# Optimization experiments

Measured on AMD Instinct MI355X. Metric: run time of the kernel, lower is better.

## Reference

```python
import jax, jax.numpy as jnp
import numpy as np

N_NODES = 50000
N_EDGES = 1600000
IN_FEAT = 48
OUT_FEAT = 48
NUM_RELS = 8


def setup_inputs() -> dict:
    key = jax.random.key(0)
    ks = jax.random.split(key, 9)
    # xavier-ish scale for relu gain
    s1 = float(np.sqrt(2.0) * np.sqrt(6.0 / (IN_FEAT + IN_FEAT)))
    s2 = float(np.sqrt(2.0) * np.sqrt(6.0 / (IN_FEAT + OUT_FEAT)))
    return {
        "inputs": jax.random.normal(ks[0], (N_NODES, IN_FEAT), dtype=jnp.float32),
        "norm": jax.random.uniform(ks[1], (N_EDGES, 1), dtype=jnp.float32),
        "weight1": jax.random.uniform(ks[2], (NUM_RELS, IN_FEAT, IN_FEAT), jnp.float32, -s1, s1),
        "weight2": jax.random.uniform(ks[3], (NUM_RELS, IN_FEAT, OUT_FEAT), jnp.float32, -s2, s2),
        "bias1": jax.random.normal(ks[4], (IN_FEAT,), dtype=jnp.float32) * 0.1,
        "bias2": jax.random.normal(ks[5], (OUT_FEAT,), dtype=jnp.float32) * 0.1,
        "src": jax.random.randint(ks[6], (N_EDGES,), 0, N_NODES, dtype=jnp.int64) if jax.config.jax_enable_x64 else jax.random.randint(ks[6], (N_EDGES,), 0, N_NODES).astype(jnp.int32),
        "dst": jax.random.randint(ks[7], (N_EDGES,), 0, N_NODES).astype(jnp.int32),
        "rel_type": jax.random.randint(ks[8], (N_EDGES,), 0, NUM_RELS).astype(jnp.int32),
    }


def reference(inputs, norm, weight1, weight2, bias1, bias2, src, dst, rel_type):
    # Message depends only on (src node, relation): precompute per (node, rel).
    # Stage 1: h1[n,r,:] = relu(h[n] @ W1[r] + b1)   -> [N, R, in]
    h1 = jax.nn.relu(jnp.einsum('ni,rij->nrj', inputs, weight1) + bias1)
    # Stage 2: h2[n,r,:] = h1[n,r] @ W2[r]           -> [N, R, out]
    h2 = jnp.einsum('nrj,rjo->nro', h1, weight2)
    # Per-edge gather + norm scaling                 -> [E, out]
    msg = h2[src, rel_type] * norm
    # Scatter-sum aggregation to destination nodes   -> [N, out]
    agg = jax.ops.segment_sum(msg, dst, num_segments=inputs.shape[0])
    # apply_func: bias2 + activation
    return jax.nn.relu(agg + bias2)
```

## Files before the change

### kernel.cpp

```cpp
#include <hip/hip_runtime.h>

#define NN 50000
#define EE 1600000
#define FF 48
#define RR 8
#define H2_ROW 64
#define LSTR 72
#define NSEG 8
#define SCAP 16

#define WB 8

#define H2TILES 391
#define H2BLKS (H2TILES * RR)
#define K2GRID (H2BLKS * 3)

typedef __attribute__((ext_vector_type(8))) short frag8;
typedef __attribute__((ext_vector_type(4))) float frag4f;

__device__ inline unsigned short bf16r(float f) {
    unsigned u = __float_as_uint(f);
    return (unsigned short)((u + 0x7FFFu + ((u >> 16) & 1u)) >> 16);
}
__device__ inline unsigned bf16pack2(float a, float b) {
    return (unsigned)bf16r(a) | ((unsigned)bf16r(b) << 16);
}
__device__ inline frag8 pack8(float4 a, float4 b) {
    union { frag8 f; unsigned u[4]; } r;
    r.u[0] = bf16pack2(a.x, a.y); r.u[1] = bf16pack2(a.z, a.w);
    r.u[2] = bf16pack2(b.x, b.y); r.u[3] = bf16pack2(b.z, b.w);
    return r.f;
}

__global__ __launch_bounds__(256) void pre_kernel(
    const float* __restrict__ W1, const float* __restrict__ W2,
    unsigned short* __restrict__ W1t, unsigned short* __restrict__ W2t)
{
    int r = blockIdx.x;
    const float* w1 = W1 + (size_t)r * FF * FF;
    const float* w2 = W2 + (size_t)r * FF * FF;
    for (int idx = threadIdx.x; idx < 48 * 64; idx += 256) {
        int j = idx >> 6, k = idx & 63;
        W1t[(size_t)r * 48 * 64 + idx] = (k < FF) ? bf16r(w1[k * FF + j]) : (unsigned short)0;
        W2t[(size_t)r * 48 * 64 + idx] = (k < FF) ? bf16r(w2[k * FF + j]) : (unsigned short)0;
    }
}

__global__ __launch_bounds__(256) void h2_place_kernel(
    const float* __restrict__ X, const unsigned short* __restrict__ W1t,
    const unsigned short* __restrict__ W2t, const float* __restrict__ B1,
    const int* __restrict__ srcv, const int* __restrict__ dstv,
    const int* __restrict__ relv, const float* __restrict__ norm,
    int* __restrict__ count, unsigned* __restrict__ payload,
    unsigned short* __restrict__ H2)
{
    __shared__ unsigned short h1s[128 * LSTR];
    int b = blockIdx.x;
    int bmod = b - (b / 3) * 3;
    if (bmod != 0) {
        int p = (b / 3) * 2 + bmod - 1;
        int e = p * 256 + threadIdx.x;
        if (e < EE) {
            int xcd;
            asm volatile("s_getreg_b32 %0, hwreg(HW_REG_XCC_ID)" : "=s"(xcd));
            xcd &= (NSEG - 1);
            int d = dstv[e];
            unsigned qn = (unsigned)(norm[e] * 8192.0f + 0.5f);
            if (qn > 8191u) qn = 8191u;
            unsigned rec = ((unsigned)(srcv[e] * 8 + relv[e]) << 13) | qn;
            int x = xcd;
            #pragma unroll 1
            for (int attempt = 0; attempt < NSEG; ++attempt) {
                int pos = atomicAdd(&count[d * NSEG + x], 1);
                if (pos < SCAP) {
                    __builtin_nontemporal_store(
                        rec, &payload[((size_t)d * NSEG + x) * SCAP + pos]);
                    break;
                }
                x = (x + 1) & (NSEG - 1);
            }
        }
        return;
    }
    int h    = b / 3;
    int r    = h & 7;
    int tile = h >> 3;
    int tid  = threadIdx.x;
    int w    = tid >> 6, ln = tid & 63, q = ln >> 4, lq = ln & 15;
    int nb   = tile * 128 + w * 32;

    unsigned short* myh1 = &h1s[(w * 32) * LSTR];
    for (int i = ln; i < 32 * 12; i += 64) {
        int rr = i / 12, cs = i - rr * 12;
        *(unsigned*)&myh1[rr * LSTR + 48 + cs * 2] = 0;
    }

    int row0 = nb + lq;      if (row0 >= NN) row0 = NN - 1;
    int row1 = nb + 16 + lq; if (row1 >= NN) row1 = NN - 1;
    const float* x0 = X + (size_t)row0 * FF;
    const float* x1 = X + (size_t)row1 * FF;

    frag8 a00 = pack8(*(const float4*)(x0 + q * 8), *(const float4*)(x0 + q * 8 + 4));
    frag8 a10 = pack8(*(const float4*)(x1 + q * 8), *(const float4*)(x1 + q * 8 + 4));
    frag8 a01 = {0, 0, 0, 0, 0, 0, 0, 0};
    frag8 a11 = {0, 0, 0, 0, 0, 0, 0, 0};
    if (q < 2) {
        a01 = pack8(*(const float4*)(x0 + 32 + q * 8), *(const float4*)(x0 + 36 + q * 8));
        a11 = pack8(*(const float4*)(x1 + 32 + q * 8), *(const float4*)(x1 + 36 + q * 8));
    }

    const unsigned short* w1r = W1t + (size_t)r * 48 * 64;
    const unsigned short* w2r = W2t + (size_t)r * 48 * 64;

    #pragma unroll
    for (int t = 0; t < 3; ++t) {
        int col = t * 16 + lq;
        frag8 b0 = *(const frag8*)&w1r[(col << 6) + q * 8];
        frag8 b1 = *(const frag8*)&w1r[(col << 6) + 32 + q * 8];
        float bc = B1[col];
        frag4f acc0 = {bc, bc, bc, bc};
        frag4f acc1 = {bc, bc, bc, bc};
        acc0 = __builtin_amdgcn_mfma_f32_16x16x32_bf16(a00, b0, acc0, 0, 0, 0);
        acc0 = __builtin_amdgcn_mfma_f32_16x16x32_bf16(a01, b1, acc0, 0, 0, 0);
        acc1 = __builtin_amdgcn_mfma_f32_16x16x32_bf16(a10, b0, acc1, 0, 0, 0);
        acc1 = __builtin_amdgcn_mfma_f32_16x16x32_bf16(a11, b1, acc1, 0, 0, 0);
        #pragma unroll
        for (int g = 0; g < 4; ++g) {
            myh1[(q * 4 + g) * LSTR + col]      = bf16r(fmaxf(acc0[g], 0.0f));
            myh1[(16 + q * 4 + g) * LSTR + col] = bf16r(fmaxf(acc1[g], 0.0f));
        }
    }

    const frag8 c00 = *(const frag8*)&myh1[lq * LSTR + q * 8];
    const frag8 c01 = *(const frag8*)&myh1[lq * LSTR + 32 + q * 8];
    const frag8 c10 = *(const frag8*)&myh1[(16 + lq) * LSTR + q * 8];
    const frag8 c11 = *(const frag8*)&myh1[(16 + lq) * LSTR + 32 + q * 8];

    #pragma unroll
    for (int t = 0; t < 3; ++t) {
        int col = t * 16 + lq;
        frag8 b0 = *(const frag8*)&w2r[(col << 6) + q * 8];
        frag8 b1 = *(const frag8*)&w2r[(col << 6) + 32 + q * 8];
        frag4f acc0 = {0.f, 0.f, 0.f, 0.f};
        frag4f acc1 = {0.f, 0.f, 0.f, 0.f};
        acc0 = __builtin_amdgcn_mfma_f32_16x16x32_bf16(c00, b0, acc0, 0, 0, 0);
        acc0 = __builtin_amdgcn_mfma_f32_16x16x32_bf16(c01, b1, acc0, 0, 0, 0);
        acc1 = __builtin_amdgcn_mfma_f32_16x16x32_bf16(c10, b0, acc1, 0, 0, 0);
        acc1 = __builtin_amdgcn_mfma_f32_16x16x32_bf16(c11, b1, acc1, 0, 0, 0);
        #pragma unroll
        for (int g = 0; g < 4; ++g) {
            int n0 = nb + q * 4 + g;
            int n1 = nb + 16 + q * 4 + g;
            if (n0 < NN) H2[((size_t)n0 * RR + r) * H2_ROW + col] = bf16r(acc0[g]);
            if (n1 < NN) H2[((size_t)n1 * RR + r) * H2_ROW + col] = bf16r(acc1[g]);
        }
    }
}

__global__ __launch_bounds__(256) void gather_kernel(
    const unsigned short* __restrict__ H2, const unsigned* __restrict__ payload,
    const int* __restrict__ count, const float* __restrict__ B2,
    float* __restrict__ out)
{
    unsigned tid = blockIdx.x * 256u + threadIdx.x;
    unsigned n = tid / 12u;
    unsigned c = tid - n * 12u;
    if (n >= NN) return;

    int4 ca = ((const int4*)(count + (size_t)n * NSEG))[0];
    int4 cb = ((const int4*)(count + (size_t)n * NSEG))[1];
    int c0 = min(ca.x, SCAP), c1 = min(ca.y, SCAP);
    int c2 = min(ca.z, SCAP), c3 = min(ca.w, SCAP);
    int c4 = min(cb.x, SCAP), c5 = min(cb.y, SCAP);
    int c6 = min(cb.z, SCAP), c7 = min(cb.w, SCAP);
    int p1 = c0, p2 = p1 + c1, p3 = p2 + c2, p4 = p3 + c3;
    int p5 = p4 + c4, p6 = p5 + c5, p7 = p6 + c6;
    int total = p7 + c7;
    const unsigned* pl = payload + (size_t)n * (NSEG * SCAP);

    auto slot = [&](int idx) -> unsigned {
        int x, base;
        if (idx < p4) {
            if (idx < p2) { x = (idx < p1) ? 0 : 1; base = (idx < p1) ? 0 : p1; }
            else          { x = (idx < p3) ? 2 : 3; base = (idx < p3) ? p2 : p3; }
        } else {
            if (idx < p6) { x = (idx < p5) ? 4 : 5; base = (idx < p5) ? p4 : p5; }
            else          { x = (idx < p7) ? 6 : 7; base = (idx < p7) ? p6 : p7; }
        }
        return pl[x * SCAP + (idx - base)];
    };

    float a0 = 0.f, a1 = 0.f, a2 = 0.f, a3 = 0.f;
    int e = 0;
    for (; e + 8 <= total; e += 8) {
        unsigned p[8];
        #pragma unroll
        for (int k = 0; k < 8; ++k) p[k] = slot(e + k);
        uint2 v[8];
        #pragma unroll
        for (int k = 0; k < 8; ++k)
            v[k] = ((const uint2*)(H2 + (size_t)(p[k] >> 13) * H2_ROW))[c];
        #pragma unroll
        for (int k = 0; k < 8; ++k) {
            float nm = (float)(p[k] & 8191u) * (1.0f / 8192.0f);
            a0 = fmaf(__uint_as_float(v[k].x << 16),         nm, a0);
            a1 = fmaf(__uint_as_float(v[k].x & 0xFFFF0000u), nm, a1);
            a2 = fmaf(__uint_as_float(v[k].y << 16),         nm, a2);
            a3 = fmaf(__uint_as_float(v[k].y & 0xFFFF0000u), nm, a3);
        }
    }
    for (; e < total; ++e) {
        unsigned p = slot(e);
        float nm = (float)(p & 8191u) * (1.0f / 8192.0f);
        uint2 v = ((const uint2*)(H2 + (size_t)(p >> 13) * H2_ROW))[c];
        a0 = fmaf(__uint_as_float(v.x << 16),         nm, a0);
        a1 = fmaf(__uint_as_float(v.x & 0xFFFF0000u), nm, a1);
        a2 = fmaf(__uint_as_float(v.y << 16),         nm, a2);
        a3 = fmaf(__uint_as_float(v.y & 0xFFFF0000u), nm, a3);
    }
    float4 b = ((const float4*)B2)[c];
    ((float4*)out)[(size_t)n * 12u + c] = make_float4(
        fmaxf(a0 + b.x, 0.f), fmaxf(a1 + b.y, 0.f),
        fmaxf(a2 + b.z, 0.f), fmaxf(a3 + b.w, 0.f));
}

extern "C" void kernel_launch(void* const* d_in, const int* in_sizes, int n_in,
                              void* d_out, int out_size, void* d_ws, size_t ws_size,
                              hipStream_t stream) {
    const float* X   = (const float*)d_in[0];
    const float* nrm = (const float*)d_in[1];
    const float* W1  = (const float*)d_in[2];
    const float* W2  = (const float*)d_in[3];
    const float* B1  = (const float*)d_in[4];
    const float* B2  = (const float*)d_in[5];
    const int*   src = (const int*)d_in[6];
    const int*   dst = (const int*)d_in[7];
    const int*   rel = (const int*)d_in[8];
    float* out = (float*)d_out;

    unsigned short* H2      = (unsigned short*)d_ws;
    unsigned*       payload = (unsigned*)(H2 + (size_t)NN * RR * H2_ROW);
    unsigned short* W1t     = (unsigned short*)(payload + (size_t)NN * NSEG * SCAP);
    unsigned short* W2t     = W1t + RR * 48 * 64;
    int*            count   = (int*)(W2t + RR * 48 * 64);

    hipMemsetAsync(count, 0, (size_t)NN * NSEG * sizeof(int), stream);

    pre_kernel<<<WB, 256, 0, stream>>>(W1, W2, W1t, W2t);

    h2_place_kernel<<<K2GRID, 256, 0, stream>>>(
        X, W1t, W2t, B1, src, dst, rel, nrm, count, payload, H2);

    unsigned total = (unsigned)NN * 12u;
    gather_kernel<<<(total + 255) / 256, 256, 0, stream>>>(
        H2, payload, count, B2, out);
}
```

Before: 218.0 us.

## Use XCD-major count/payload layout, fold count zeroing into pre kernel

The per-node segment counters and payload slots move from node-major to XCD-segment-major, so that atomics issued from one XCD land in a contiguous region, presumably to reduce cross-XCD cache-line contention. The memset is replaced by extra blocks in pre_kernel that zero the counters, which removes one launch. H2 stores become nontemporal and payload stores become regular stores. The gather now reads eight strided count words per node instead of two int4 loads, which costs coalescing and locality on the read side.

```diff
diff --git a/kernel.cpp b/kernel.cpp
--- a/kernel.cpp
+++ b/kernel.cpp
@@ -10,6 +10,8 @@
 #define SCAP 16
 
 #define WB 8
+#define ZB 391
+#define K1GRID (WB + ZB)
 
 #define H2TILES 391
 #define H2BLKS (H2TILES * RR)
@@ -34,16 +36,23 @@
 
 __global__ __launch_bounds__(256) void pre_kernel(
     const float* __restrict__ W1, const float* __restrict__ W2,
-    unsigned short* __restrict__ W1t, unsigned short* __restrict__ W2t)
+    unsigned short* __restrict__ W1t, unsigned short* __restrict__ W2t,
+    int* __restrict__ count)
 {
-    int r = blockIdx.x;
-    const float* w1 = W1 + (size_t)r * FF * FF;
-    const float* w2 = W2 + (size_t)r * FF * FF;
-    for (int idx = threadIdx.x; idx < 48 * 64; idx += 256) {
-        int j = idx >> 6, k = idx & 63;
-        W1t[(size_t)r * 48 * 64 + idx] = (k < FF) ? bf16r(w1[k * FF + j]) : (unsigned short)0;
-        W2t[(size_t)r * 48 * 64 + idx] = (k < FF) ? bf16r(w2[k * FF + j]) : (unsigned short)0;
-    }
+    int b = blockIdx.x;
+    if (b < WB) {
+        int r = b;
+        const float* w1 = W1 + (size_t)r * FF * FF;
+        const float* w2 = W2 + (size_t)r * FF * FF;
+        for (int idx = threadIdx.x; idx < 48 * 64; idx += 256) {
+            int j = idx >> 6, k = idx & 63;
+            W1t[(size_t)r * 48 * 64 + idx] = (k < FF) ? bf16r(w1[k * FF + j]) : (unsigned short)0;
+            W2t[(size_t)r * 48 * 64 + idx] = (k < FF) ? bf16r(w2[k * FF + j]) : (unsigned short)0;
+        }
+        return;
+    }
+    int z = (b - WB) * 256 + threadIdx.x;
+    if (z < 100000) ((int4*)count)[z] = make_int4(0, 0, 0, 0);
 }
 
 __global__ __launch_bounds__(256) void h2_place_kernel(
@@ -71,10 +80,9 @@
             int x = xcd;
             #pragma unroll 1
             for (int attempt = 0; attempt < NSEG; ++attempt) {
-                int pos = atomicAdd(&count[d * NSEG + x], 1);
+                int pos = atomicAdd(&count[x * NN + d], 1);
                 if (pos < SCAP) {
-                    __builtin_nontemporal_store(
-                        rec, &payload[((size_t)d * NSEG + x) * SCAP + pos]);
+                    payload[((size_t)x * NN + d) * SCAP + pos] = rec;
                     break;
                 }
                 x = (x + 1) & (NSEG - 1);
@@ -151,8 +159,12 @@
         for (int g = 0; g < 4; ++g) {
             int n0 = nb + q * 4 + g;
             int n1 = nb + 16 + q * 4 + g;
-            if (n0 < NN) H2[((size_t)n0 * RR + r) * H2_ROW + col] = bf16r(acc0[g]);
-            if (n1 < NN) H2[((size_t)n1 * RR + r) * H2_ROW + col] = bf16r(acc1[g]);
+            if (n0 < NN)
+                __builtin_nontemporal_store(bf16r(acc0[g]),
+                    &H2[((size_t)n0 * RR + r) * H2_ROW + col]);
+            if (n1 < NN)
+                __builtin_nontemporal_store(bf16r(acc1[g]),
+                    &H2[((size_t)n1 * RR + r) * H2_ROW + col]);
         }
     }
 }
@@ -167,16 +179,13 @@
     unsigned c = tid - n * 12u;
     if (n >= NN) return;
 
-    int4 ca = ((const int4*)(count + (size_t)n * NSEG))[0];
-    int4 cb = ((const int4*)(count + (size_t)n * NSEG))[1];
-    int c0 = min(ca.x, SCAP), c1 = min(ca.y, SCAP);
-    int c2 = min(ca.z, SCAP), c3 = min(ca.w, SCAP);
-    int c4 = min(cb.x, SCAP), c5 = min(cb.y, SCAP);
-    int c6 = min(cb.z, SCAP), c7 = min(cb.w, SCAP);
-    int p1 = c0, p2 = p1 + c1, p3 = p2 + c2, p4 = p3 + c3;
-    int p5 = p4 + c4, p6 = p5 + c5, p7 = p6 + c6;
-    int total = p7 + c7;
-    const unsigned* pl = payload + (size_t)n * (NSEG * SCAP);
+    int cx[NSEG];
+    #pragma unroll
+    for (int x = 0; x < NSEG; ++x) cx[x] = min(count[(size_t)x * NN + n], SCAP);
+    int p1 = cx[0], p2 = p1 + cx[1], p3 = p2 + cx[2], p4 = p3 + cx[3];
+    int p5 = p4 + cx[4], p6 = p5 + cx[5], p7 = p6 + cx[6];
+    int total = p7 + cx[7];
+    const unsigned* pl = payload + (size_t)n * SCAP;
 
     auto slot = [&](int idx) -> unsigned {
         int x, base;
@@ -187,7 +196,7 @@
             if (idx < p6) { x = (idx < p5) ? 4 : 5; base = (idx < p5) ? p4 : p5; }
             else          { x = (idx < p7) ? 6 : 7; base = (idx < p7) ? p6 : p7; }
         }
-        return pl[x * SCAP + (idx - base)];
+        return pl[(size_t)x * (NN * SCAP) + (idx - base)];
     };
 
     float a0 = 0.f, a1 = 0.f, a2 = 0.f, a3 = 0.f;
@@ -244,9 +253,7 @@
     unsigned short* W2t     = W1t + RR * 48 * 64;
     int*            count   = (int*)(W2t + RR * 48 * 64);
 
-    hipMemsetAsync(count, 0, (size_t)NN * NSEG * sizeof(int), stream);
-
-    pre_kernel<<<WB, 256, 0, stream>>>(W1, W2, W1t, W2t);
+    pre_kernel<<<K1GRID, 256, 0, stream>>>(W1, W2, W1t, W2t, count);
 
     h2_place_kernel<<<K2GRID, 256, 0, stream>>>(
         X, W1t, W2t, B1, src, dst, rel, nrm, count, payload, H2);
```

Result: no change. 214.7 us, median of 2 (-1.5%).
